# Kernel tuning notes

Measured on AMD Instinct MI355X. Metric: run time of the kernel, lower is better.

## Reference

```python
import jax, jax.numpy as jnp
import numpy as np

N, E = 50000, 500000
IN_C, HID, OUT_C, HEADS, NL = 128, 16, 16, 8, 4
EPS = 1e-5
NEG_SLOPE = 0.2


def _gatv2(x, src, dst, Wl, Wr, att, bias, concat):
    # GATv2Conv (PyG semantics, eval mode): lin_l on source, lin_r on target,
    # e = a . LeakyReLU(xl[src] + xr[dst]); segment softmax over dst; scatter-sum.
    n = x.shape[0]
    H, C = att.shape
    xl = (x @ Wl).reshape(n, H, C)
    xr = (x @ Wr).reshape(n, H, C)
    e = jax.nn.leaky_relu(xl[src] + xr[dst], NEG_SLOPE)          # [E', H, C]
    logit = jnp.einsum('ehc,hc->eh', e, att)                      # [E', H]
    mx = jax.lax.stop_gradient(jax.ops.segment_max(logit, dst, num_segments=n))
    a = jnp.exp(logit - mx[dst])
    denom = jax.ops.segment_sum(a, dst, num_segments=n)
    alpha = a / denom[dst]                                        # [E', H]
    out = jax.ops.segment_sum(xl[src] * alpha[..., None], dst, num_segments=n)
    out = out.reshape(n, H * C) if concat else out.mean(axis=1)
    return out + bias


def _bn_eval(x, g, b, m, v):
    return (x - m) * jax.lax.rsqrt(v + EPS) * g + b


def setup_inputs() -> dict:
    key = jax.random.key(0)
    ks = jax.random.split(key, 32)
    d = {}
    d['x'] = jax.random.normal(ks[0], (N, IN_C), dtype=jnp.float32)
    d['edge_index'] = jax.random.randint(ks[1], (2, E), 0, N, dtype=jnp.int64)
    HC = HID * HEADS  # 128
    dims_in = [IN_C, HC, HC, HC]
    dims_h = [HEADS, HEADS, HEADS, 1]
    dims_c = [HID, HID, HID, OUT_C]
    ki = 2
    for i in range(NL):
        fan = dims_in[i]
        s = 1.0 / np.sqrt(fan)
        d[f'W{i}l'] = jax.random.uniform(ks[ki], (fan, dims_h[i] * dims_c[i]), minval=-s, maxval=s, dtype=jnp.float32); ki += 1
        d[f'W{i}r'] = jax.random.uniform(ks[ki], (fan, dims_h[i] * dims_c[i]), minval=-s, maxval=s, dtype=jnp.float32); ki += 1
        d[f'a{i}'] = jax.random.normal(ks[ki], (dims_h[i], dims_c[i]), dtype=jnp.float32) * 0.1; ki += 1
        out_dim = dims_h[i] * dims_c[i] if i < NL - 1 else dims_c[i]
        d[f'b{i}'] = jnp.zeros((out_dim,), dtype=jnp.float32)
    for i in range(NL - 1):
        d[f'g{i}'] = jnp.ones((HC,), dtype=jnp.float32) + 0.1 * jax.random.normal(ks[ki], (HC,), dtype=jnp.float32); ki += 1
        d[f'be{i}'] = 0.1 * jax.random.normal(ks[ki], (HC,), dtype=jnp.float32); ki += 1
        d[f'm{i}'] = 0.1 * jax.random.normal(ks[ki], (HC,), dtype=jnp.float32); ki += 1
        d[f'v{i}'] = jnp.ones((HC,), dtype=jnp.float32)
    return d


def reference(x, edge_index, W0l, W0r, a0, b0, W1l, W1r, a1, b1, W2l, W2r, a2, b2, W3l, W3r, a3, b3, g0, be0, m0, v0, g1, be1, m1, v1, g2, be2, m2, v2):
    n = x.shape[0]
    loop = jnp.arange(n, dtype=edge_index.dtype)
    src = jnp.concatenate([edge_index[0], loop])  # add_self_loops=True (PyG default)
    dst = jnp.concatenate([edge_index[1], loop])
    Ws = [(W0l, W0r, a0, b0), (W1l, W1r, a1, b1), (W2l, W2r, a2, b2), (W3l, W3r, a3, b3)]
    bns = [(g0, be0, m0, v0), (g1, be1, m1, v1), (g2, be2, m2, v2)]
    h = x
    for i in range(NL):
        Wl, Wr, att, bias = Ws[i]
        h = _gatv2(h, src, dst, Wl, Wr, att, bias, concat=(i < NL - 1))
        if i < NL - 1:
            g, b, m, v = bns[i]
            h = jax.nn.elu(_bn_eval(h, g, b, m, v))
    return h
```

## Files before the change

kernel.cpp:

```cpp
#include <hip/hip_runtime.h>
#include <hip/hip_fp16.h>
#include <math.h>

static constexpr float BN_EPS = 1e-5f;
static constexpr float NEG = 0.2f;

typedef short s16x8 __attribute__((ext_vector_type(8)));
typedef float f32x4 __attribute__((ext_vector_type(4)));
typedef _Float16 h16x2 __attribute__((ext_vector_type(2)));

__device__ inline unsigned short f2bf(float f) {
    unsigned int u = __float_as_uint(f);
    unsigned int r = (u + 0x7fffu + ((u >> 16) & 1u)) >> 16;
    return (unsigned short)r;
}
__device__ inline float bf2f(unsigned short h) {
    return __uint_as_float(((unsigned int)h) << 16);
}


__global__ void hist_kernel(const int* __restrict__ ei, int E, int n, int* __restrict__ cnt) {
    int e = blockIdx.x * blockDim.x + threadIdx.x;
    int ET = E + n;
    if (e >= ET) return;
    int d = (e < E) ? ei[E + e] : (e - E);
    atomicAdd(&cnt[d], 1);
}

__global__ void scan_block(const int* __restrict__ cnt, int* __restrict__ rowptr,
                           int* __restrict__ bsums, int n) {
    __shared__ int s[1024];
    int i = blockIdx.x * 1024 + threadIdx.x;
    int vv = (i < n) ? cnt[i] : 0;
    s[threadIdx.x] = vv;
    __syncthreads();
    for (int d = 1; d < 1024; d <<= 1) {
        int t = (threadIdx.x >= d) ? s[threadIdx.x - d] : 0;
        __syncthreads();
        s[threadIdx.x] += t;
        __syncthreads();
    }
    if (i < n) rowptr[i + 1] = s[threadIdx.x];
    if (threadIdx.x == 1023) bsums[blockIdx.x] = s[1023];
}

__global__ void scan_bsums(int* __restrict__ bsums, int nb) {
    int L = threadIdx.x;
    int v = (L < nb) ? bsums[L] : 0;
    for (int d = 1; d < 64; d <<= 1) {
        int t = __shfl_up(v, d);
        if (L >= d) v += t;
    }
    int ex = __shfl_up(v, 1);
    if (L == 0) ex = 0;
    if (L < nb) bsums[L] = ex;
}

__global__ void scan_add(int* __restrict__ rowptr, const int* __restrict__ bsums, int n) {
    int i = blockIdx.x * 1024 + threadIdx.x;
    if (i < n) rowptr[i + 1] += bsums[blockIdx.x];
    if (i == 0) rowptr[0] = 0;
}

__global__ void scatter_kernel(const int* __restrict__ ei, int E, int n,
                               const int* __restrict__ rowptr, int* __restrict__ fill,
                               int* __restrict__ col) {
    int e = blockIdx.x * blockDim.x + threadIdx.x;
    int ET = E + n;
    if (e >= ET) return;
    int s, d;
    if (e < E) { s = ei[e]; d = ei[E + e]; } else { s = e - E; d = s; }
    int pos = atomicAdd(&fill[d], 1);
    col[rowptr[d] + pos] = s;
}


__global__ void convert_split(const float* __restrict__ x, unsigned short* __restrict__ hi,
                              unsigned short* __restrict__ lo, int total4) {
    int i = blockIdx.x * blockDim.x + threadIdx.x;
    if (i >= total4) return;
    float4 v = *(const float4*)&x[(size_t)i * 4];
    float vs[4] = {v.x, v.y, v.z, v.w};
    unsigned short h[4], l[4];
#pragma unroll
    for (int j = 0; j < 4; j++) {
        h[j] = f2bf(vs[j]);
        l[j] = f2bf(vs[j] - bf2f(h[j]));
    }
    *(ushort4*)&hi[(size_t)i * 4] = make_ushort4(h[0], h[1], h[2], h[3]);
    *(ushort4*)&lo[(size_t)i * 4] = make_ushort4(l[0], l[1], l[2], l[3]);
}


__global__ void pack_w(const float* __restrict__ Wl, const float* __restrict__ Wr,
                       unsigned short* __restrict__ packed, int M, int NTT) {
    int tile = blockIdx.x;
    int NT = NTT >> 1;
    int gnt = tile % NTT;
    int kt = tile / NTT;
    int l = threadIdx.x;
    const float* W = (gnt < NT) ? Wl : Wr;
    int col = (gnt % NT) * 16 + (l & 15);
    int krow = kt * 32 + ((l >> 4) << 3);
    size_t base = (size_t)tile * 1024 + (size_t)l * 8;
#pragma unroll
    for (int j = 0; j < 8; j++) {
        float v = W[(size_t)(krow + j) * M + col];
        unsigned short h = f2bf(v);
        packed[base + j] = h;
        packed[base + 512 + j] = f2bf(v - bf2f(h));
    }
}


__global__ __launch_bounds__(256) void gemm_mfma_big(
    const unsigned short* __restrict__ xhi, const unsigned short* __restrict__ xlo,
    const unsigned short* __restrict__ packed,
    __half* __restrict__ Y1, __half* __restrict__ Y2, int n) {
    __shared__ unsigned short sA[2][64 * 136];
    const int t = threadIdx.x;
    const int row0 = blockIdx.x * 64;

    for (int c = t; c < 1024; c += 256) {
        int row = c >> 4;
        int off = (c & 15) * 8;
        int gr = row0 + row;
        if (gr >= n) gr = n - 1;
        *(s16x8*)&sA[0][row * 136 + off] = *(const s16x8*)&xhi[(size_t)gr * 128 + off];
        *(s16x8*)&sA[1][row * 136 + off] = *(const s16x8*)&xlo[(size_t)gr * 128 + off];
    }
    __syncthreads();

    const int lane = t & 63;
    const int s = t >> 6;
    const int lr = lane & 15;
    const int kq = (lane >> 4) * 8;

    s16x8 ahi[4][4], alo[4][4];
#pragma unroll
    for (int rt = 0; rt < 4; rt++)
#pragma unroll
        for (int kt = 0; kt < 4; kt++) {
            int addr = (rt * 16 + lr) * 136 + kt * 32 + kq;
            ahi[rt][kt] = *(const s16x8*)&sA[0][addr];
            alo[rt][kt] = *(const s16x8*)&sA[1][addr];
        }

    f32x4 acc[4][4];
#pragma unroll
    for (int a = 0; a < 4; a++)
#pragma unroll
        for (int b = 0; b < 4; b++) acc[a][b] = (f32x4){0.f, 0.f, 0.f, 0.f};

#pragma unroll
    for (int kt = 0; kt < 4; kt++) {
#pragma unroll
        for (int ntl = 0; ntl < 4; ntl++) {
            int nt = s * 4 + ntl;
            const unsigned short* pb = packed + ((size_t)(kt * 16 + nt)) * 1024 + lane * 8;
            s16x8 bhi = *(const s16x8*)pb;
            s16x8 blo = *(const s16x8*)(pb + 512);
#pragma unroll
            for (int rt = 0; rt < 4; rt++) {
                acc[ntl][rt] = __builtin_amdgcn_mfma_f32_16x16x32_bf16(ahi[rt][kt], bhi, acc[ntl][rt], 0, 0, 0);
                acc[ntl][rt] = __builtin_amdgcn_mfma_f32_16x16x32_bf16(alo[rt][kt], bhi, acc[ntl][rt], 0, 0, 0);
                acc[ntl][rt] = __builtin_amdgcn_mfma_f32_16x16x32_bf16(ahi[rt][kt], blo, acc[ntl][rt], 0, 0, 0);
            }
        }
    }

    __half* Y = (s < 2) ? Y1 : Y2;
    const int colh = (s & 1) * 64;
    const int rq = (lane >> 4) * 4;
#pragma unroll
    for (int ntl = 0; ntl < 4; ntl++) {
        int col = colh + ntl * 16 + lr;
#pragma unroll
        for (int rt = 0; rt < 4; rt++) {
#pragma unroll
            for (int g = 0; g < 4; g++) {
                int row = row0 + rt * 16 + rq + g;
                if (row < n) Y[(size_t)row * 128 + col] = __float2half(acc[ntl][rt][g]);
            }
        }
    }
}


template <int NTT>
__global__ __launch_bounds__(256) void gemm_mfma(const unsigned short* __restrict__ xhi,
                                                 const unsigned short* __restrict__ xlo,
                                                 const unsigned short* __restrict__ packed,
                                                 float* __restrict__ Y1, float* __restrict__ Y2,
                                                 int n) {
    constexpr int NT = NTT / 2;
    constexpr int M = NT * 16;
    int lane = threadIdx.x & 63;
    int wv = blockIdx.x * 4 + (threadIdx.x >> 6);
    int row0 = wv * 16;
    if (row0 >= n) return;
    int r = row0 + (lane & 15);
    if (r >= n) r = n - 1;
    int kq = (lane >> 4) * 8;

    s16x8 ahi[4], alo[4];
#pragma unroll
    for (int kt = 0; kt < 4; kt++) {
        ahi[kt] = *(const s16x8*)&xhi[(size_t)r * 128 + kt * 32 + kq];
        alo[kt] = *(const s16x8*)&xlo[(size_t)r * 128 + kt * 32 + kq];
    }

    f32x4 acc[NTT];
#pragma unroll
    for (int nt = 0; nt < NTT; nt++) acc[nt] = (f32x4){0.f, 0.f, 0.f, 0.f};

#pragma unroll
    for (int kt = 0; kt < 4; kt++) {
#pragma unroll
        for (int nt = 0; nt < NTT; nt++) {
            const unsigned short* pb = packed + ((size_t)(kt * NTT + nt)) * 1024 + lane * 8;
            s16x8 bhi = *(const s16x8*)pb;
            s16x8 blo = *(const s16x8*)(pb + 512);
            acc[nt] = __builtin_amdgcn_mfma_f32_16x16x32_bf16(ahi[kt], bhi, acc[nt], 0, 0, 0);
            acc[nt] = __builtin_amdgcn_mfma_f32_16x16x32_bf16(alo[kt], bhi, acc[nt], 0, 0, 0);
            acc[nt] = __builtin_amdgcn_mfma_f32_16x16x32_bf16(ahi[kt], blo, acc[nt], 0, 0, 0);
        }
    }

    int colb = lane & 15;
    int rbase = row0 + (lane >> 4) * 4;
#pragma unroll
    for (int nt = 0; nt < NTT; nt++) {
        float* Y = (nt < NT) ? Y1 : Y2;
        int col = (nt % NT) * 16 + colb;
#pragma unroll
        for (int g = 0; g < 4; g++) {
            int row = rbase + g;
            if (row < n) Y[(size_t)row * M + col] = acc[nt][g];
        }
    }
}


__device__ __forceinline__ float dot4_h(h16x2 l01, h16x2 l23,
                                        h16x2 a01, h16x2 a23) {
#if __has_builtin(__builtin_amdgcn_fdot2)
    float part = __builtin_amdgcn_fdot2(l01, a01, 0.f, false);
    return __builtin_amdgcn_fdot2(l23, a23, part, false);
#else
    return fmaf((float)l01.x, (float)a01.x, fmaf((float)l01.y, (float)a01.y,
           fmaf((float)l23.x, (float)a23.x, (float)l23.y * (float)a23.y)));
#endif
}

__global__ __launch_bounds__(256) void agg_h(
    const __half* __restrict__ xl, const __half* __restrict__ xr,
    const int* __restrict__ rowptr, const int* __restrict__ col,
    const float* __restrict__ att, const float* __restrict__ bias,
    const float* __restrict__ g, const float* __restrict__ be,
    const float* __restrict__ bm, const float* __restrict__ bv,
    unsigned short* __restrict__ ohi, unsigned short* __restrict__ olo, int n) {
    int v = (blockIdx.x * blockDim.x + threadIdx.x) >> 6;
    if (v >= n) return;
    int lane = threadIdx.x & 63;
    int half = lane >> 5;
    int L = lane & 31;
    int ch = 4 * L;

    float2 rraw = *(const float2*)&xr[(size_t)v * 128 + ch];
    h16x2 rx01 = *(h16x2*)&rraw.x;
    h16x2 rx23 = *(h16x2*)&rraw.y;
    float4 av = *(const float4*)&att[ch];
    h16x2 a01 = {(_Float16)av.x, (_Float16)av.y};
    h16x2 a23 = {(_Float16)av.z, (_Float16)av.w};
    const h16x2 neg2 = {(_Float16)NEG, (_Float16)NEG};

    int beg = rowptr[v];
    int end = rowptr[v + 1];

    float lrun = 0.f;
    float4 acc = make_float4(0.f, 0.f, 0.f, 0.f);

    auto proc = [&](float2 raw, bool ok) {
        h16x2 h01 = *(h16x2*)&raw.x;
        h16x2 h23 = *(h16x2*)&raw.y;
        h16x2 s01 = h01 + rx01;
        h16x2 s23 = h23 + rx23;
        h16x2 l01 = __builtin_elementwise_max(s01, s01 * neg2);
        h16x2 l23 = __builtin_elementwise_max(s23, s23 * neg2);
        float part = dot4_h(l01, l23, a01, a23);
        part += __shfl_xor(part, 1);
        part += __shfl_xor(part, 2);
        float p = ok ? __expf(part) : 0.f;
        lrun += p;
        acc.x = fmaf(p, (float)h01.x, acc.x);
        acc.y = fmaf(p, (float)h01.y, acc.y);
        acc.z = fmaf(p, (float)h23.x, acc.z);
        acc.w = fmaf(p, (float)h23.y, acc.w);
    };

    int e = beg;
    for (; e + 8 <= end; e += 8) {
        float2 r[4];
#pragma unroll
        for (int j = 0; j < 4; j++) {
            int u = col[e + 2 * j + half];
            r[j] = *(const float2*)&xl[((size_t)u << 7) + ch];
        }
#pragma unroll
        for (int j = 0; j < 4; j++) proc(r[j], true);
    }
    for (; e < end; e += 4) {
        float2 r[2];
        bool ok[2];
#pragma unroll
        for (int j = 0; j < 2; j++) {
            int idx = e + 2 * j + half;
            ok[j] = (idx < end);
            r[j] = make_float2(0.f, 0.f);
            if (ok[j]) {
                int u = col[idx];
                r[j] = *(const float2*)&xl[((size_t)u << 7) + ch];
            }
        }
#pragma unroll
        for (int j = 0; j < 2; j++) proc(r[j], ok[j]);
    }

    lrun += __shfl_xor(lrun, 32);
    acc.x += __shfl_xor(acc.x, 32);
    acc.y += __shfl_xor(acc.y, 32);
    acc.z += __shfl_xor(acc.z, 32);
    acc.w += __shfl_xor(acc.w, 32);

    if (half == 0) {
        float inv = 1.0f / lrun;
        float4 b4 = *(const float4*)&bias[ch];
        float o[4] = {fmaf(acc.x, inv, b4.x), fmaf(acc.y, inv, b4.y),
                      fmaf(acc.z, inv, b4.z), fmaf(acc.w, inv, b4.w)};
        float4 m4 = *(const float4*)&bm[ch];
        float4 v4 = *(const float4*)&bv[ch];
        float4 g4 = *(const float4*)&g[ch];
        float4 e4 = *(const float4*)&be[ch];
        float ms[4] = {m4.x, m4.y, m4.z, m4.w};
        float vs[4] = {v4.x, v4.y, v4.z, v4.w};
        float gs[4] = {g4.x, g4.y, g4.z, g4.w};
        float es[4] = {e4.x, e4.y, e4.z, e4.w};
        unsigned short h[4], l2[4];
#pragma unroll
        for (int j = 0; j < 4; j++) {
            o[j] = (o[j] - ms[j]) * rsqrtf(vs[j] + BN_EPS) * gs[j] + es[j];
            o[j] = o[j] > 0.f ? o[j] : expm1f(o[j]);
            h[j] = f2bf(o[j]);
            l2[j] = f2bf(o[j] - bf2f(h[j]));
        }
        *(ushort4*)&ohi[(size_t)v * 128 + ch] = make_ushort4(h[0], h[1], h[2], h[3]);
        *(ushort4*)&olo[(size_t)v * 128 + ch] = make_ushort4(l2[0], l2[1], l2[2], l2[3]);
    }
}


__global__ __launch_bounds__(256) void agg_f(
    const float* __restrict__ xl, const float* __restrict__ xr,
    const int* __restrict__ rowptr, const int* __restrict__ col,
    const float* __restrict__ att, const float* __restrict__ bias,
    float* __restrict__ out, int n) {
    int v = (blockIdx.x * blockDim.x + threadIdx.x) >> 6;
    if (v >= n) return;
    int lane = threadIdx.x & 63;
    int slot = lane >> 2;
    int L = lane & 3;
    int ch = 4 * L;

    float4 xrv = *(const float4*)&xr[(size_t)v * 16 + ch];
    float4 av = *(const float4*)&att[ch];
    int beg = rowptr[v];
    int end = rowptr[v + 1];

    float lrun = 0.f;
    float4 acc = make_float4(0.f, 0.f, 0.f, 0.f);

    for (int eb = beg; eb < end; eb += 16) {
        int idx = eb + slot;
        bool ok = (idx < end);
        float4 xv = make_float4(0.f, 0.f, 0.f, 0.f);
        if (ok) {
            int u = col[idx];
            xv = *(const float4*)&xl[((size_t)u << 4) + ch];
        }
        float s0 = xv.x + xrv.x; s0 = s0 > 0.f ? s0 : NEG * s0;
        float s1 = xv.y + xrv.y; s1 = s1 > 0.f ? s1 : NEG * s1;
        float s2 = xv.z + xrv.z; s2 = s2 > 0.f ? s2 : NEG * s2;
        float s3 = xv.w + xrv.w; s3 = s3 > 0.f ? s3 : NEG * s3;
        float part = fmaf(s0, av.x, fmaf(s1, av.y, fmaf(s2, av.z, s3 * av.w)));
        part += __shfl_xor(part, 1);
        part += __shfl_xor(part, 2);
        float p = ok ? __expf(part) : 0.f;
        lrun += p;
        acc.x = fmaf(p, xv.x, acc.x);
        acc.y = fmaf(p, xv.y, acc.y);
        acc.z = fmaf(p, xv.z, acc.z);
        acc.w = fmaf(p, xv.w, acc.w);
    }

#pragma unroll
    for (int d = 4; d < 64; d <<= 1) {
        lrun += __shfl_xor(lrun, d);
        acc.x += __shfl_xor(acc.x, d);
        acc.y += __shfl_xor(acc.y, d);
        acc.z += __shfl_xor(acc.z, d);
        acc.w += __shfl_xor(acc.w, d);
    }

    if (slot == 0) {
        float inv = 1.0f / lrun;
        float4 b4 = *(const float4*)&bias[ch];
        *(float4*)&out[(size_t)v * 16 + ch] =
            make_float4(fmaf(acc.x, inv, b4.x), fmaf(acc.y, inv, b4.y),
                        fmaf(acc.z, inv, b4.z), fmaf(acc.w, inv, b4.w));
    }
}


extern "C" void kernel_launch(void* const* d_in, const int* in_sizes, int n_in,
                              void* d_out, int out_size, void* d_ws, size_t ws_size,
                              hipStream_t stream) {
    const float* x = (const float*)d_in[0];
    const int* ei = (const int*)d_in[1];
    const float* Wl[4] = {(const float*)d_in[2], (const float*)d_in[6],
                          (const float*)d_in[10], (const float*)d_in[14]};
    const float* Wr[4] = {(const float*)d_in[3], (const float*)d_in[7],
                          (const float*)d_in[11], (const float*)d_in[15]};
    const float* att[4] = {(const float*)d_in[4], (const float*)d_in[8],
                           (const float*)d_in[12], (const float*)d_in[16]};
    const float* bias[4] = {(const float*)d_in[5], (const float*)d_in[9],
                            (const float*)d_in[13], (const float*)d_in[17]};
    const float* g[3] = {(const float*)d_in[18], (const float*)d_in[22], (const float*)d_in[26]};
    const float* be[3] = {(const float*)d_in[19], (const float*)d_in[23], (const float*)d_in[27]};
    const float* bm[3] = {(const float*)d_in[20], (const float*)d_in[24], (const float*)d_in[28]};
    const float* bv[3] = {(const float*)d_in[21], (const float*)d_in[25], (const float*)d_in[29]};

    const int n = in_sizes[0] / 128;
    const int E = in_sizes[1] / 2;
    const int ET = E + n;

    char* p = (char*)d_ws;
    __half* xlh = (__half*)p;          p += (size_t)n * 128 * 2;
    __half* xrh = (__half*)p;          p += (size_t)n * 128 * 2;
    float* xl3 = (float*)p;            p += (size_t)n * 16 * 4;
    float* xr3 = (float*)p;            p += (size_t)n * 16 * 4;
    unsigned short* xhi = (unsigned short*)p;  p += (size_t)n * 128 * 2;
    unsigned short* xlo = (unsigned short*)p;  p += (size_t)n * 128 * 2;
    int* rowptr = (int*)p;            p += (size_t)(n + 1) * 4;
    int* cnt = (int*)p;               p += (size_t)n * 4;
    int* fill = (int*)p;              p += (size_t)n * 4;
    int* col = (int*)p;               p += (size_t)ET * 4;
    int* bsums = (int*)p;             p += 256;
    unsigned short* pk[4];
    for (int i = 0; i < 3; i++) { pk[i] = (unsigned short*)p; p += 4 * 16 * 1024 * 2; }
    pk[3] = (unsigned short*)p;       p += 4 * 2 * 1024 * 2;

    (void)hipMemsetAsync(cnt, 0, (size_t)n * 4, stream);
    (void)hipMemsetAsync(fill, 0, (size_t)n * 4, stream);

    const int tb = 256;
    hist_kernel<<<(ET + tb - 1) / tb, tb, 0, stream>>>(ei, E, n, cnt);
    int nb = (n + 1023) / 1024;
    scan_block<<<nb, 1024, 0, stream>>>(cnt, rowptr, bsums, n);
    scan_bsums<<<1, 64, 0, stream>>>(bsums, nb);
    scan_add<<<nb, 1024, 0, stream>>>(rowptr, bsums, n);
    scatter_kernel<<<(ET + tb - 1) / tb, tb, 0, stream>>>(ei, E, n, rowptr, fill, col);

    convert_split<<<(n * 32 + 255) / 256, 256, 0, stream>>>(x, xhi, xlo, n * 32);
    for (int i = 0; i < 3; i++)
        pack_w<<<4 * 16, 64, 0, stream>>>(Wl[i], Wr[i], pk[i], 128, 16);
    pack_w<<<4 * 2, 64, 0, stream>>>(Wl[3], Wr[3], pk[3], 16, 2);

    const int gb64 = (n + 63) / 64;
    const int gemmBlocksSmall = ((n + 15) / 16 + 3) / 4;
    const int aggBlocks = (n + 3) / 4;

    for (int i = 0; i < 3; i++) {
        gemm_mfma_big<<<gb64, 256, 0, stream>>>(xhi, xlo, pk[i], xlh, xrh, n);
        agg_h<<<aggBlocks, 256, 0, stream>>>(
            xlh, xrh, rowptr, col, att[i], bias[i], g[i], be[i], bm[i], bv[i],
            xhi, xlo, n);
    }
    gemm_mfma<2><<<gemmBlocksSmall, 256, 0, stream>>>(xhi, xlo, pk[3], xl3, xr3, n);
    agg_f<<<aggBlocks, 256, 0, stream>>>(
        xl3, xr3, rowptr, col, att[3], bias[3], (float*)d_out, n);
}
```

Baseline: 409.5 us.

## Remap agg_h lanes to one head per lane with 8 edges per wave

The per-edge work in the fp16 aggregation kernel is reorganised so each lane owns a full 16-channel head and processes one of 8 edges at a time, instead of 4 channels across two edges. The head logit now comes from eight in-lane dot products with no per-edge cross-lane shuffles, and each lane issues two 16-byte gathers per edge. The cost is 16 float accumulators per lane, a larger cross-slot shuffle reduction at the end (3 rounds over 17 values), and lanes sitting idle on nodes whose degree is not a multiple of 8.

```diff
diff --git a/kernel.cpp b/kernel.cpp
--- a/kernel.cpp
+++ b/kernel.cpp
@@ -242,14 +242,13 @@
 }
 
 
-__device__ __forceinline__ float dot4_h(h16x2 l01, h16x2 l23,
-                                        h16x2 a01, h16x2 a23) {
+struct H8 { h16x2 a, b, c, d; };
+
+__device__ __forceinline__ float fdot2w(h16x2 x, h16x2 y, float init) {
 #if __has_builtin(__builtin_amdgcn_fdot2)
-    float part = __builtin_amdgcn_fdot2(l01, a01, 0.f, false);
-    return __builtin_amdgcn_fdot2(l23, a23, part, false);
+    return __builtin_amdgcn_fdot2(x, y, init, false);
 #else
-    return fmaf((float)l01.x, (float)a01.x, fmaf((float)l01.y, (float)a01.y,
-           fmaf((float)l23.x, (float)a23.x, (float)l23.y * (float)a23.y)));
+    return fmaf((float)x.x, (float)y.x, fmaf((float)x.y, (float)y.y, init));
 #endif
 }
 
@@ -263,99 +262,113 @@
     int v = (blockIdx.x * blockDim.x + threadIdx.x) >> 6;
     if (v >= n) return;
     int lane = threadIdx.x & 63;
-    int half = lane >> 5;
-    int L = lane & 31;
-    int ch = 4 * L;
-
-    float2 rraw = *(const float2*)&xr[(size_t)v * 128 + ch];
-    h16x2 rx01 = *(h16x2*)&rraw.x;
-    h16x2 rx23 = *(h16x2*)&rraw.y;
-    float4 av = *(const float4*)&att[ch];
-    h16x2 a01 = {(_Float16)av.x, (_Float16)av.y};
-    h16x2 a23 = {(_Float16)av.z, (_Float16)av.w};
+    int slot = lane >> 3;
+    int head = lane & 7;
+    int ch = head * 16;
+
+    const __half* xrp = &xr[(size_t)v * 128 + ch];
+    H8 rx0 = *(const H8*)xrp;
+    H8 rx1 = *(const H8*)(xrp + 8);
+    H8 a0, a1;
+    {
+        float4 f0 = *(const float4*)&att[ch];
+        float4 f1 = *(const float4*)&att[ch + 4];
+        float4 f2 = *(const float4*)&att[ch + 8];
+        float4 f3 = *(const float4*)&att[ch + 12];
+        a0.a = (h16x2){(_Float16)f0.x, (_Float16)f0.y};
+        a0.b = (h16x2){(_Float16)f0.z, (_Float16)f0.w};
+        a0.c = (h16x2){(_Float16)f1.x, (_Float16)f1.y};
+        a0.d = (h16x2){(_Float16)f1.z, (_Float16)f1.w};
+        a1.a = (h16x2){(_Float16)f2.x, (_Float16)f2.y};
+        a1.b = (h16x2){(_Float16)f2.z, (_Float16)f2.w};
+        a1.c = (h16x2){(_Float16)f3.x, (_Float16)f3.y};
+        a1.d = (h16x2){(_Float16)f3.z, (_Float16)f3.w};
+    }
     const h16x2 neg2 = {(_Float16)NEG, (_Float16)NEG};
 
     int beg = rowptr[v];
     int end = rowptr[v + 1];
 
     float lrun = 0.f;
-    float4 acc = make_float4(0.f, 0.f, 0.f, 0.f);
-
-    auto proc = [&](float2 raw, bool ok) {
-        h16x2 h01 = *(h16x2*)&raw.x;
-        h16x2 h23 = *(h16x2*)&raw.y;
-        h16x2 s01 = h01 + rx01;
-        h16x2 s23 = h23 + rx23;
-        h16x2 l01 = __builtin_elementwise_max(s01, s01 * neg2);
-        h16x2 l23 = __builtin_elementwise_max(s23, s23 * neg2);
-        float part = dot4_h(l01, l23, a01, a23);
-        part += __shfl_xor(part, 1);
-        part += __shfl_xor(part, 2);
+    float acc[16];
+#pragma unroll
+    for (int k = 0; k < 16; k++) acc[k] = 0.f;
+
+    for (int eb = beg; eb < end; eb += 8) {
+        int idx = eb + slot;
+        bool ok = (idx < end);
+        H8 x0 = {{0,0},{0,0},{0,0},{0,0}};
+        H8 x1 = {{0,0},{0,0},{0,0},{0,0}};
+        if (ok) {
+            int u = col[idx];
+            const __half* src = &xl[((size_t)u << 7) + ch];
+            x0 = *(const H8*)src;
+            x1 = *(const H8*)(src + 8);
+        }
+        h16x2 s;
+        float part = 0.f;
+        s = x0.a + rx0.a; part = fdot2w(__builtin_elementwise_max(s, s * neg2), a0.a, part);
+        s = x0.b + rx0.b; part = fdot2w(__builtin_elementwise_max(s, s * neg2), a0.b, part);
+        s = x0.c + rx0.c; part = fdot2w(__builtin_elementwise_max(s, s * neg2), a0.c, part);
+        s = x0.d + rx0.d; part = fdot2w(__builtin_elementwise_max(s, s * neg2), a0.d, part);
+        s = x1.a + rx1.a; part = fdot2w(__builtin_elementwise_max(s, s * neg2), a1.a, part);
+        s = x1.b + rx1.b; part = fdot2w(__builtin_elementwise_max(s, s * neg2), a1.b, part);
+        s = x1.c + rx1.c; part = fdot2w(__builtin_elementwise_max(s, s * neg2), a1.c, part);
+        s = x1.d + rx1.d; part = fdot2w(__builtin_elementwise_max(s, s * neg2), a1.d, part);
         float p = ok ? __expf(part) : 0.f;
         lrun += p;
-        acc.x = fmaf(p, (float)h01.x, acc.x);
-        acc.y = fmaf(p, (float)h01.y, acc.y);
-        acc.z = fmaf(p, (float)h23.x, acc.z);
-        acc.w = fmaf(p, (float)h23.y, acc.w);
-    };
-
-    int e = beg;
-    for (; e + 8 <= end; e += 8) {
-        float2 r[4];
-#pragma unroll
-        for (int j = 0; j < 4; j++) {
-            int u = col[e + 2 * j + half];
-            r[j] = *(const float2*)&xl[((size_t)u << 7) + ch];
-        }
-#pragma unroll
-        for (int j = 0; j < 4; j++) proc(r[j], true);
-    }
-    for (; e < end; e += 4) {
-        float2 r[2];
-        bool ok[2];
-#pragma unroll
-        for (int j = 0; j < 2; j++) {
-            int idx = e + 2 * j + half;
-            ok[j] = (idx < end);
-            r[j] = make_float2(0.f, 0.f);
-            if (ok[j]) {
-                int u = col[idx];
-                r[j] = *(const float2*)&xl[((size_t)u << 7) + ch];
+        acc[0]  = fmaf(p, (float)x0.a.x, acc[0]);
+        acc[1]  = fmaf(p, (float)x0.a.y, acc[1]);
+        acc[2]  = fmaf(p, (float)x0.b.x, acc[2]);
+        acc[3]  = fmaf(p, (float)x0.b.y, acc[3]);
+        acc[4]  = fmaf(p, (float)x0.c.x, acc[4]);
+        acc[5]  = fmaf(p, (float)x0.c.y, acc[5]);
+        acc[6]  = fmaf(p, (float)x0.d.x, acc[6]);
+        acc[7]  = fmaf(p, (float)x0.d.y, acc[7]);
+        acc[8]  = fmaf(p, (float)x1.a.x, acc[8]);
+        acc[9]  = fmaf(p, (float)x1.a.y, acc[9]);
+        acc[10] = fmaf(p, (float)x1.b.x, acc[10]);
+        acc[11] = fmaf(p, (float)x1.b.y, acc[11]);
+        acc[12] = fmaf(p, (float)x1.c.x, acc[12]);
+        acc[13] = fmaf(p, (float)x1.c.y, acc[13]);
+        acc[14] = fmaf(p, (float)x1.d.x, acc[14]);
+        acc[15] = fmaf(p, (float)x1.d.y, acc[15]);
+    }
+
+#pragma unroll
+    for (int d = 8; d < 64; d <<= 1) {
+        lrun += __shfl_xor(lrun, d);
+#pragma unroll
+        for (int k = 0; k < 16; k++) acc[k] += __shfl_xor(acc[k], d);
+    }
+
+    if (slot == 0) {
+        float inv = 1.0f / lrun;
+#pragma unroll
+        for (int q = 0; q < 4; q++) {
+            int c4 = ch + q * 4;
+            float4 b4 = *(const float4*)&bias[c4];
+            float4 m4 = *(const float4*)&bm[c4];
+            float4 v4 = *(const float4*)&bv[c4];
+            float4 g4 = *(const float4*)&g[c4];
+            float4 e4 = *(const float4*)&be[c4];
+            float bs[4] = {b4.x, b4.y, b4.z, b4.w};
+            float ms[4] = {m4.x, m4.y, m4.z, m4.w};
+            float vs[4] = {v4.x, v4.y, v4.z, v4.w};
+            float gs[4] = {g4.x, g4.y, g4.z, g4.w};
+            float es[4] = {e4.x, e4.y, e4.z, e4.w};
+            unsigned short h[4], l2[4];
+#pragma unroll
+            for (int j = 0; j < 4; j++) {
+                float o = fmaf(acc[q * 4 + j], inv, bs[j]);
+                o = (o - ms[j]) * rsqrtf(vs[j] + BN_EPS) * gs[j] + es[j];
+                o = o > 0.f ? o : expm1f(o);
+                h[j] = f2bf(o);
+                l2[j] = f2bf(o - bf2f(h[j]));
             }
-        }
-#pragma unroll
-        for (int j = 0; j < 2; j++) proc(r[j], ok[j]);
-    }
-
-    lrun += __shfl_xor(lrun, 32);
-    acc.x += __shfl_xor(acc.x, 32);
-    acc.y += __shfl_xor(acc.y, 32);
-    acc.z += __shfl_xor(acc.z, 32);
-    acc.w += __shfl_xor(acc.w, 32);
-
-    if (half == 0) {
-        float inv = 1.0f / lrun;
-        float4 b4 = *(const float4*)&bias[ch];
-        float o[4] = {fmaf(acc.x, inv, b4.x), fmaf(acc.y, inv, b4.y),
-                      fmaf(acc.z, inv, b4.z), fmaf(acc.w, inv, b4.w)};
-        float4 m4 = *(const float4*)&bm[ch];
-        float4 v4 = *(const float4*)&bv[ch];
-        float4 g4 = *(const float4*)&g[ch];
-        float4 e4 = *(const float4*)&be[ch];
-        float ms[4] = {m4.x, m4.y, m4.z, m4.w};
-        float vs[4] = {v4.x, v4.y, v4.z, v4.w};
-        float gs[4] = {g4.x, g4.y, g4.z, g4.w};
-        float es[4] = {e4.x, e4.y, e4.z, e4.w};
-        unsigned short h[4], l2[4];
-#pragma unroll
-        for (int j = 0; j < 4; j++) {
-            o[j] = (o[j] - ms[j]) * rsqrtf(vs[j] + BN_EPS) * gs[j] + es[j];
-            o[j] = o[j] > 0.f ? o[j] : expm1f(o[j]);
-            h[j] = f2bf(o[j]);
-            l2[j] = f2bf(o[j] - bf2f(h[j]));
-        }
-        *(ushort4*)&ohi[(size_t)v * 128 + ch] = make_ushort4(h[0], h[1], h[2], h[3]);
-        *(ushort4*)&olo[(size_t)v * 128 + ch] = make_ushort4(l2[0], l2[1], l2[2], l2[3]);
+            *(ushort4*)&ohi[(size_t)v * 128 + c4] = make_ushort4(h[0], h[1], h[2], h[3]);
+            *(ushort4*)&olo[(size_t)v * 128 + c4] = make_ushort4(l2[0], l2[1], l2[2], l2[3]);
+        }
     }
 }
 
```

Result: slower. 522.3 us (+27.6%).
